# Performance work log

Hardware: AMD Instinct MI355X
Metric: run time of the kernel (lower is better)

Reference implementation:

```python
import jax, jax.numpy as jnp
import numpy as np

EMB = 512
NUM_HEAD = 8
HEAD_DIM = EMB // NUM_HEAD  # 64
B, S = 16, 2048


def setup_inputs() -> dict:
    key = jax.random.key(0)
    k1, k2, k3, k4 = jax.random.split(key, 4)
    x1 = jax.random.normal(k1, (B, S, EMB), dtype=jnp.float32)
    # causal mask: 1 where attention allowed, 0 elsewhere (masked_fill where mask==0)
    mask = jnp.tril(jnp.ones((S, S), dtype=jnp.int32))
    scale = 1.0 / np.sqrt(EMB)
    Wq = jax.random.normal(k2, (EMB, HEAD_DIM), dtype=jnp.float32) * scale
    Wk = jax.random.normal(k3, (EMB, HEAD_DIM), dtype=jnp.float32) * scale
    Wv = jax.random.normal(k4, (EMB, HEAD_DIM), dtype=jnp.float32) * scale
    return {"x1": x1, "mask": mask, "Wq": Wq, "Wk": Wk, "Wv": Wv}


def reference(x1, mask, Wq, Wk, Wv):
    # q,k,v: [B,S,H]
    q = jnp.einsum('bse,eh->bsh', x1, Wq)
    k = jnp.einsum('bse,eh->bsh', x1, Wk)
    v = jnp.einsum('bse,eh->bsh', x1, Wv)
    # scores: [B,S,S]
    scaled_qk = jnp.einsum('bqh,bkh->bqk', q, k) / jnp.sqrt(jnp.float32(HEAD_DIM))
    scaled_qk = jnp.where(mask == 0, -jnp.inf, scaled_qk)
    attn = jax.nn.softmax(scaled_qk, axis=-1)
    return jnp.einsum('bqk,bkh->bqh', attn, v)
```

## Files before the change

kernel.cpp:

```cpp
#include <hip/hip_runtime.h>
#include <hip/hip_bf16.h>

typedef __attribute__((ext_vector_type(8))) short bf16x8;
typedef __attribute__((ext_vector_type(4))) float f32x4;
typedef __attribute__((ext_vector_type(4))) unsigned short u16x4;

#define MFMA16(a, b, c) __builtin_amdgcn_mfma_f32_16x16x32_bf16(a, b, c, 0, 0, 0)

#define QSCALE 0.18033688011112042f

#define GLDS16(gp, lp)                                                         \
    __builtin_amdgcn_global_load_lds(                                          \
        (const __attribute__((address_space(1))) void*)(gp),                   \
        (__attribute__((address_space(3))) void*)(lp), 16, 0, 0)

__device__ __forceinline__ short nbf(float f) {
    __hip_bfloat16 h = __float2bfloat16(f);
    return *(short*)&h;
}
__device__ __forceinline__ unsigned short nbfu(float f) {
    __hip_bfloat16 h = __float2bfloat16(f);
    return *(unsigned short*)&h;
}

__global__ void wt_kernel(const float* __restrict__ Wq, const float* __restrict__ Wk,
                          const float* __restrict__ Wv, unsigned short* __restrict__ Wt) {
    const int h = blockIdx.x;
    const int mat = blockIdx.y;
    const int e = threadIdx.x;
    const float* W = (mat == 0) ? Wq : ((mat == 1) ? Wk : Wv);
    Wt[(mat * 64 + h) * 512 + e] = nbfu(W[e * 64 + h]);
}

__global__ __launch_bounds__(256, 2) void qkv_proj(
    const float* __restrict__ x1, const unsigned short* __restrict__ Wt,
    unsigned short* __restrict__ Q, unsigned short* __restrict__ K,
    unsigned short* __restrict__ Vt)
{
    __shared__ char alds[2][8192];
    __shared__ char blds[2][12288];

    const int tid = threadIdx.x;
    const int w = tid >> 6, lane = tid & 63;
    const int c = lane & 15, g = lane >> 4;
    const int tokB = blockIdx.x * 64;

    const char* x1b = (const char*)x1;
    const char* Wtb = (const char*)Wt;

    const int tA0 = tid >> 3,           qA0 = (tid & 7) ^ (tA0 & 7);
    const int tA1 = (tid + 256) >> 3,   qA1 = (tid & 7) ^ (tA1 & 7);
    const size_t aoff0 = (size_t)(tokB + tA0) * 2048 + qA0 * 16;
    const size_t aoff1 = (size_t)(tokB + tA1) * 2048 + qA1 * 16;

    auto bsrc = [&](int j) -> size_t {
        const int n = j >> 6, c2 = (j >> 2) & 15, g2 = j & 3;
        return (size_t)((n >> 2) * 64 + (n & 3) * 16 + c2) * 1024 + g2 * 16;
    };
    const size_t boff0 = bsrc(tid), boff1 = bsrc(tid + 256), boff2 = bsrc(tid + 512);

    f32x4 acc[12];
#pragma unroll
    for (int n = 0; n < 12; ++n) acc[n] = (f32x4)0.f;

    GLDS16(x1b + aoff0, &alds[0][tid * 16]);
    GLDS16(x1b + aoff1, &alds[0][4096 + tid * 16]);
    GLDS16(Wtb + boff0, &blds[0][tid * 16]);
    GLDS16(Wtb + boff1, &blds[0][4096 + tid * 16]);
    GLDS16(Wtb + boff2, &blds[0][8192 + tid * 16]);

    const int arow = (w * 16 + c) * 128;
    const int aq0 = (((2 * g) ^ (c & 7)) * 16);
    const int aq1 = (((2 * g + 1) ^ (c & 7)) * 16);
    const int brd = (c * 4 + g) * 16;

    int buf = 0;
    for (int ks = 0; ks < 16; ++ks) {
        asm volatile("s_waitcnt vmcnt(0)\n\ts_barrier" ::: "memory");

        if (ks < 15) {
            const size_t ka = (size_t)(ks + 1) * 128;
            const size_t kb = (size_t)(ks + 1) * 64;
            char* ab = &alds[buf ^ 1][0];
            char* bb = &blds[buf ^ 1][0];
            GLDS16(x1b + aoff0 + ka, ab + tid * 16);
            GLDS16(x1b + aoff1 + ka, ab + 4096 + tid * 16);
            GLDS16(Wtb + boff0 + kb, bb + tid * 16);
            GLDS16(Wtb + boff1 + kb, bb + 4096 + tid * 16);
            GLDS16(Wtb + boff2 + kb, bb + 8192 + tid * 16);
        }

        const char* ab = &alds[buf][0];
        const char* bb = &blds[buf][0];
        f32x4 a0 = *(const f32x4*)(ab + arow + aq0);
        f32x4 a1 = *(const f32x4*)(ab + arow + aq1);
        bf16x8 af;
        af[0] = nbf(a0[0]); af[1] = nbf(a0[1]); af[2] = nbf(a0[2]); af[3] = nbf(a0[3]);
        af[4] = nbf(a1[0]); af[5] = nbf(a1[1]); af[6] = nbf(a1[2]); af[7] = nbf(a1[3]);
#pragma unroll
        for (int n = 0; n < 12; ++n) {
            bf16x8 bf = *(const bf16x8*)(bb + n * 1024 + brd);
            acc[n] = MFMA16(af, bf, acc[n]);
        }
        buf ^= 1;
    }

    const int tok0 = tokB + w * 16;
#pragma unroll
    for (int n = 0; n < 4; ++n)
#pragma unroll
        for (int r = 0; r < 4; ++r)
            Q[(size_t)(tok0 + g * 4 + r) * 64 + n * 16 + c] = nbfu(acc[n][r] * QSCALE);
#pragma unroll
    for (int n = 0; n < 4; ++n)
#pragma unroll
        for (int r = 0; r < 4; ++r)
            K[(size_t)(tok0 + g * 4 + r) * 64 + n * 16 + c] = nbfu(acc[4 + n][r]);

    const int b = tok0 >> 11;
    const int sl = (tok0 & 2047) + g * 4;
#pragma unroll
    for (int n = 0; n < 4; ++n) {
        const int d = n * 16 + c;
        u16x4 pv;
#pragma unroll
        for (int r = 0; r < 4; ++r) pv[r] = nbfu(acc[8 + n][r]);
        *(u16x4*)(Vt + ((size_t)(b * 64 + d) << 11) + sl) = pv;
    }
}

__global__ __launch_bounds__(512, 1) void flash_attn(
    const unsigned short* __restrict__ Q, const unsigned short* __restrict__ K,
    const unsigned short* __restrict__ Vt, float* __restrict__ out)
{
    __shared__ char kv[2][65536];
    __shared__ char p_lds[32768];

    const int tid = threadIdx.x;
    const int W = tid >> 6;
    const int st = W >> 2;
    const int w = W & 3;
    const int lane = tid & 63;
    const int c = lane & 15, g = lane >> 4;

    const int id = blockIdx.x;
    const int b = 2 * (id & 7) + ((id >> 3) & 1);
    const int qt = 31 - (id >> 4);
    const int n2 = (qt >> 1) + 1;
    const int J = (n2 + 1) >> 1;
    const int qr0c = qt * 64 + w * 16 + c;
    const size_t qrow_g = ((size_t)b << 11) + qt * 64 + w * 16;

    bf16x8 qf0 = *(const bf16x8*)(Q + (qrow_g + c) * 64 + g * 8);
    bf16x8 qf1 = *(const bf16x8*)(Q + (qrow_g + c) * 64 + 32 + g * 8);

    const char* Kb = (const char*)(K + (((size_t)b << 11) * 64));
    const char* Vb = (const char*)(Vt + (((size_t)b << 11) * 64));

    const int c2 = tid & 15, g2 = (tid >> 4) & 3, nn = (tid >> 6) & 3, s4 = (tid >> 8) & 1;
    const int koff = (nn * 16 + c2) * 128 + g2 * 16 + s4 * 64;
    const int voff = (nn * 16 + c2) * 4096 + g2 * 16 + s4 * 64;

    float m = -1e30f, l = 0.f;
    f32x4 acc[4];
#pragma unroll
    for (int n = 0; n < 4; ++n) acc[n] = (f32x4)0.f;

    {
        char* d = &kv[0][0];
        GLDS16(Kb + koff,                 d + tid * 16);
        GLDS16(Kb + koff + 8192,          d + 8192 + tid * 16);
        GLDS16(Vb + voff,                 d + 16384 + tid * 16);
        GLDS16(Vb + voff + 128,           d + 16384 + 8192 + tid * 16);
        GLDS16(Kb + 16384 + koff,         d + 32768 + tid * 16);
        GLDS16(Kb + 16384 + koff + 8192,  d + 32768 + 8192 + tid * 16);
        GLDS16(Vb + 256 + voff,           d + 49152 + tid * 16);
        GLDS16(Vb + 256 + voff + 128,     d + 49152 + 8192 + tid * 16);
    }

    for (int j = 0; j < J; ++j) {
        asm volatile("s_waitcnt vmcnt(0)\n\ts_barrier" ::: "memory");

        if (j + 1 < J) {
            const size_t kA = (size_t)(2 * j + 2) * 16384;
            const size_t vA = (size_t)(2 * j + 2) * 256;
            char* d = &kv[(j & 1) ^ 1][0];
            GLDS16(Kb + kA + koff,                 d + tid * 16);
            GLDS16(Kb + kA + koff + 8192,          d + 8192 + tid * 16);
            GLDS16(Vb + vA + voff,                 d + 16384 + tid * 16);
            GLDS16(Vb + vA + voff + 128,           d + 16384 + 8192 + tid * 16);
            GLDS16(Kb + kA + 16384 + koff,         d + 32768 + tid * 16);
            GLDS16(Kb + kA + 16384 + koff + 8192,  d + 32768 + 8192 + tid * 16);
            GLDS16(Vb + vA + 256 + voff,           d + 49152 + tid * 16);
            GLDS16(Vb + vA + 256 + voff + 128,     d + 49152 + 8192 + tid * 16);
        }

        const int t = 2 * j + st;
        if (t < n2) {
            const char* kb = &kv[j & 1][st * 32768];
            const char* vb = kb + 16384;

            f32x4 s[8];
#pragma unroll
            for (int i = 0; i < 8; ++i) s[i] = (f32x4)0.f;
            __builtin_amdgcn_s_setprio(1);
#pragma unroll
            for (int h = 0; h < 2; ++h)
#pragma unroll
                for (int n = 0; n < 4; ++n) {
                    bf16x8 ka0 = *(const bf16x8*)(kb + h * 8192 + n * 1024 + lane * 16);
                    bf16x8 ka1 = *(const bf16x8*)(kb + h * 8192 + 4096 + n * 1024 + lane * 16);
                    s[h * 4 + n] = MFMA16(ka0, qf0, s[h * 4 + n]);
                    s[h * 4 + n] = MFMA16(ka1, qf1, s[h * 4 + n]);
                }
            __builtin_amdgcn_s_setprio(0);

            if (t == n2 - 1) {
#pragma unroll
                for (int h = 0; h < 2; ++h)
#pragma unroll
                    for (int n = 0; n < 4; ++n) {
                        const int key0 = t * 128 + h * 64 + n * 16 + g * 4;
#pragma unroll
                        for (int r = 0; r < 4; ++r)
                            if (key0 + r > qr0c) s[h * 4 + n][r] = -1e30f;
                    }
            }

            float tm = -1e30f;
#pragma unroll
            for (int i = 0; i < 8; ++i)
                tm = fmaxf(tm, fmaxf(fmaxf(s[i][0], s[i][1]), fmaxf(s[i][2], s[i][3])));

            if (__any(tm > m + 8.f)) {
                float gm = tm;
                gm = fmaxf(gm, __shfl_xor(gm, 16, 64));
                gm = fmaxf(gm, __shfl_xor(gm, 32, 64));
                const float mn = fmaxf(m, gm);
                const float alpha = exp2f(m - mn);
                m = mn;
                l *= alpha;
                float al[4];
#pragma unroll
                for (int r = 0; r < 4; ++r) al[r] = __shfl(alpha, g * 4 + r, 16);
#pragma unroll
                for (int n = 0; n < 4; ++n)
#pragma unroll
                    for (int r = 0; r < 4; ++r) acc[n][r] *= al[r];
            }

            char* pw = &p_lds[W * 4096 + ((g >> 1) * 16 + c) * 16 + (g & 1) * 8];
#pragma unroll
            for (int h = 0; h < 2; ++h)
#pragma unroll
                for (int n = 0; n < 4; ++n) {
                    const int i = h * 4 + n;
                    float p0 = exp2f(s[i][0] - m);
                    float p1 = exp2f(s[i][1] - m);
                    float p2 = exp2f(s[i][2] - m);
                    float p3 = exp2f(s[i][3] - m);
                    l += (p0 + p1) + (p2 + p3);
                    u16x4 pk;
                    pk[0] = nbfu(p0); pk[1] = nbfu(p1); pk[2] = nbfu(p2); pk[3] = nbfu(p3);
                    *(u16x4*)(pw + (h * 2 + (n >> 1)) * 1024 + (n & 1) * 512) = pk;
                }

            const char* pr = &p_lds[W * 4096 + lane * 16];
            bf16x8 pf[4];
#pragma unroll
            for (int ps = 0; ps < 4; ++ps) pf[ps] = *(const bf16x8*)(pr + ps * 1024);
            __builtin_amdgcn_s_setprio(1);
#pragma unroll
            for (int n = 0; n < 4; ++n) {
#pragma unroll
                for (int ps = 0; ps < 4; ++ps) {
                    bf16x8 vf = *(const bf16x8*)(vb + (ps >> 1) * 8192 + (ps & 1) * 4096 + n * 1024 + lane * 16);
                    acc[n] = MFMA16(pf[ps], vf, acc[n]);
                }
            }
            __builtin_amdgcn_s_setprio(0);
        }
    }

    __syncthreads();
    float* accb = (float*)&kv[0][0];
    float* mb = (float*)&kv[0][16384];
    float* lb = (float*)&kv[0][16384 + 256];

    if (st == 1) {
        l += __shfl_xor(l, 16, 64);
        l += __shfl_xor(l, 32, 64);
        if (g == 0) { mb[w * 16 + c] = m; lb[w * 16 + c] = l; }
#pragma unroll
        for (int n = 0; n < 4; ++n)
#pragma unroll
            for (int r = 0; r < 4; ++r)
                accb[w * 1024 + (g * 4 + r) * 64 + n * 16 + c] = acc[n][r];
    }
    __syncthreads();

    if (st == 0) {
        l += __shfl_xor(l, 16, 64);
        l += __shfl_xor(l, 32, 64);
        const float m1c = mb[w * 16 + c];
        const float l1c = lb[w * 16 + c];
        const float mF = fmaxf(m, m1c);
        const float a0 = exp2f(m - mF);
        const float a1 = (m1c > -1e29f) ? exp2f(m1c - mF) : 0.f;
        const float inv = 1.f / (l * a0 + l1c * a1);
        const float s0 = a0 * inv, s1 = a1 * inv;
        float s0r[4], s1r[4];
#pragma unroll
        for (int r = 0; r < 4; ++r) {
            s0r[r] = __shfl(s0, g * 4 + r, 16);
            s1r[r] = __shfl(s1, g * 4 + r, 16);
        }
#pragma unroll
        for (int n = 0; n < 4; ++n)
#pragma unroll
            for (int r = 0; r < 4; ++r) {
                const float a1v = accb[w * 1024 + (g * 4 + r) * 64 + n * 16 + c];
                out[(qrow_g + g * 4 + r) * 64 + n * 16 + c] = acc[n][r] * s0r[r] + a1v * s1r[r];
            }
    }
}

extern "C" void kernel_launch(void* const* d_in, const int* in_sizes, int n_in,
                              void* d_out, int out_size, void* d_ws, size_t ws_size,
                              hipStream_t stream) {
    const float* x1 = (const float*)d_in[0];
    const float* Wq = (const float*)d_in[2];
    const float* Wk = (const float*)d_in[3];
    const float* Wv = (const float*)d_in[4];
    float* out = (float*)d_out;

    unsigned short* Wt  = (unsigned short*)d_ws;
    unsigned short* Qw  = (unsigned short*)((char*)d_ws + 196608);
    unsigned short* Kw  = (unsigned short*)((char*)d_ws + 196608 + 4194304);
    unsigned short* Vtw = (unsigned short*)((char*)d_ws + 196608 + 2 * 4194304);

    wt_kernel<<<dim3(64, 3), 512, 0, stream>>>(Wq, Wk, Wv, Wt);
    qkv_proj<<<512, 256, 0, stream>>>(x1, Wt, Qw, Kw, Vtw);
    flash_attn<<<512, 512, 0, stream>>>(Qw, Kw, Vtw, out);
}
```

Before: 66.21 us.

## Load K fragments directly from global and skew PV for second stream into next iteration

K tiles are no longer staged in LDS; each wave reads its K fragments straight from global memory into registers before the QK MFMAs. Only V is staged, now in a triple-buffered LDS ring. The second wave group's PV accumulation is deferred by one iteration so that it overlaps with the next tile's QK work, with a drain step after the loop. This cuts LDS traffic and footprint but adds global-load latency on the critical QK path. It also relies on the P buffer in LDS staying valid across the barrier until the deferred PV reads it.

```diff
diff --git a/kernel.cpp b/kernel.cpp
--- a/kernel.cpp
+++ b/kernel.cpp
@@ -133,7 +133,7 @@
     const unsigned short* __restrict__ Q, const unsigned short* __restrict__ K,
     const unsigned short* __restrict__ Vt, float* __restrict__ out)
 {
-    __shared__ char kv[2][65536];
+    __shared__ char vb3[3][32768];
     __shared__ char p_lds[32768];
 
     const int tid = threadIdx.x;
@@ -158,7 +158,6 @@
     const char* Vb = (const char*)(Vt + (((size_t)b << 11) * 64));
 
     const int c2 = tid & 15, g2 = (tid >> 4) & 3, nn = (tid >> 6) & 3, s4 = (tid >> 8) & 1;
-    const int koff = (nn * 16 + c2) * 128 + g2 * 16 + s4 * 64;
     const int voff = (nn * 16 + c2) * 4096 + g2 * 16 + s4 * 64;
 
     float m = -1e30f, l = 0.f;
@@ -166,53 +165,63 @@
 #pragma unroll
     for (int n = 0; n < 4; ++n) acc[n] = (f32x4)0.f;
 
-    {
-        char* d = &kv[0][0];
-        GLDS16(Kb + koff,                 d + tid * 16);
-        GLDS16(Kb + koff + 8192,          d + 8192 + tid * 16);
-        GLDS16(Vb + voff,                 d + 16384 + tid * 16);
-        GLDS16(Vb + voff + 128,           d + 16384 + 8192 + tid * 16);
-        GLDS16(Kb + 16384 + koff,         d + 32768 + tid * 16);
-        GLDS16(Kb + 16384 + koff + 8192,  d + 32768 + 8192 + tid * 16);
-        GLDS16(Vb + 256 + voff,           d + 49152 + tid * 16);
-        GLDS16(Vb + 256 + voff + 128,     d + 49152 + 8192 + tid * 16);
-    }
+    auto STAGE = [&](int p) {
+        char* d = &vb3[p % 3][0];
+        const int tA = (2 * p     < n2) ? 2 * p     : n2 - 1;
+        const int tB = (2 * p + 1 < n2) ? 2 * p + 1 : n2 - 1;
+        const size_t oa = (size_t)tA * 256, ob = (size_t)tB * 256;
+        GLDS16(Vb + oa + voff,        d + tid * 16);
+        GLDS16(Vb + oa + voff + 128,  d + 8192 + tid * 16);
+        GLDS16(Vb + ob + voff,        d + 16384 + tid * 16);
+        GLDS16(Vb + ob + voff + 128,  d + 16384 + 8192 + tid * 16);
+    };
+
+    auto PV = [&](const char* vbase) {
+        const char* pr = &p_lds[W * 4096 + lane * 16];
+        bf16x8 pf[4];
+#pragma unroll
+        for (int ps = 0; ps < 4; ++ps) pf[ps] = *(const bf16x8*)(pr + ps * 1024);
+        __builtin_amdgcn_s_setprio(1);
+#pragma unroll
+        for (int n = 0; n < 4; ++n) {
+#pragma unroll
+            for (int ps = 0; ps < 4; ++ps) {
+                bf16x8 vf = *(const bf16x8*)(vbase + (ps >> 1) * 8192 + (ps & 1) * 4096 + n * 1024 + lane * 16);
+                acc[n] = MFMA16(pf[ps], vf, acc[n]);
+            }
+        }
+        __builtin_amdgcn_s_setprio(0);
+    };
+
+    STAGE(0);
 
     for (int j = 0; j < J; ++j) {
         asm volatile("s_waitcnt vmcnt(0)\n\ts_barrier" ::: "memory");
-
-        if (j + 1 < J) {
-            const size_t kA = (size_t)(2 * j + 2) * 16384;
-            const size_t vA = (size_t)(2 * j + 2) * 256;
-            char* d = &kv[(j & 1) ^ 1][0];
-            GLDS16(Kb + kA + koff,                 d + tid * 16);
-            GLDS16(Kb + kA + koff + 8192,          d + 8192 + tid * 16);
-            GLDS16(Vb + vA + voff,                 d + 16384 + tid * 16);
-            GLDS16(Vb + vA + voff + 128,           d + 16384 + 8192 + tid * 16);
-            GLDS16(Kb + kA + 16384 + koff,         d + 32768 + tid * 16);
-            GLDS16(Kb + kA + 16384 + koff + 8192,  d + 32768 + 8192 + tid * 16);
-            GLDS16(Vb + vA + 256 + voff,           d + 49152 + tid * 16);
-            GLDS16(Vb + vA + 256 + voff + 128,     d + 49152 + 8192 + tid * 16);
-        }
+        if (j + 1 < J) STAGE(j + 1);
+
+        if (st == 1 && j >= 1) PV(&vb3[(j - 1) % 3][16384]);
 
         const int t = 2 * j + st;
         if (t < n2) {
-            const char* kb = &kv[j & 1][st * 32768];
-            const char* vb = kb + 16384;
-
+            const char* kt = Kb + (size_t)t * 16384;
+            bf16x8 kf[16];
+#pragma unroll
+            for (int h = 0; h < 2; ++h)
+#pragma unroll
+                for (int n = 0; n < 4; ++n) {
+                    const char* kp = kt + h * 8192 + (n * 16 + c) * 128 + g * 16;
+                    kf[(h * 4 + n) * 2]     = *(const bf16x8*)kp;
+                    kf[(h * 4 + n) * 2 + 1] = *(const bf16x8*)(kp + 64);
+                }
             f32x4 s[8];
 #pragma unroll
             for (int i = 0; i < 8; ++i) s[i] = (f32x4)0.f;
             __builtin_amdgcn_s_setprio(1);
 #pragma unroll
-            for (int h = 0; h < 2; ++h)
-#pragma unroll
-                for (int n = 0; n < 4; ++n) {
-                    bf16x8 ka0 = *(const bf16x8*)(kb + h * 8192 + n * 1024 + lane * 16);
-                    bf16x8 ka1 = *(const bf16x8*)(kb + h * 8192 + 4096 + n * 1024 + lane * 16);
-                    s[h * 4 + n] = MFMA16(ka0, qf0, s[h * 4 + n]);
-                    s[h * 4 + n] = MFMA16(ka1, qf1, s[h * 4 + n]);
-                }
+            for (int i = 0; i < 8; ++i) {
+                s[i] = MFMA16(kf[2 * i], qf0, s[i]);
+                s[i] = MFMA16(kf[2 * i + 1], qf1, s[i]);
+            }
             __builtin_amdgcn_s_setprio(0);
 
             if (t == n2 - 1) {
@@ -265,27 +274,16 @@
                     *(u16x4*)(pw + (h * 2 + (n >> 1)) * 1024 + (n & 1) * 512) = pk;
                 }
 
-            const char* pr = &p_lds[W * 4096 + lane * 16];
-            bf16x8 pf[4];
-#pragma unroll
-            for (int ps = 0; ps < 4; ++ps) pf[ps] = *(const bf16x8*)(pr + ps * 1024);
-            __builtin_amdgcn_s_setprio(1);
-#pragma unroll
-            for (int n = 0; n < 4; ++n) {
-#pragma unroll
-                for (int ps = 0; ps < 4; ++ps) {
-                    bf16x8 vf = *(const bf16x8*)(vb + (ps >> 1) * 8192 + (ps & 1) * 4096 + n * 1024 + lane * 16);
-                    acc[n] = MFMA16(pf[ps], vf, acc[n]);
-                }
-            }
-            __builtin_amdgcn_s_setprio(0);
-        }
-    }
+            if (st == 0) PV(&vb3[j % 3][0]);
+        }
+    }
+
+    if (st == 1 && (2 * J - 1) < n2) PV(&vb3[(J - 1) % 3][16384]);
 
     __syncthreads();
-    float* accb = (float*)&kv[0][0];
-    float* mb = (float*)&kv[0][16384];
-    float* lb = (float*)&kv[0][16384 + 256];
+    float* accb = (float*)&vb3[0][0];
+    float* mb = (float*)&vb3[0][16384];
+    float* lb = (float*)&vb3[0][16384 + 256];
 
     if (st == 1) {
         l += __shfl_xor(l, 16, 64);
```

New measurement: 86.92 us. 31.3% more time.
